# Optimization experiments

Hardware: AMD Instinct MI355X
Metric: run time of the kernel (lower is better)

The kernel has to match this reference:

```python
import jax, jax.numpy as jnp
import numpy as np

B, T = 256, 128
DW = 768          # dim_word
DH = 768          # dim_hidden (must equal DW per broadcast in original code)
NC = 3            # num_classification
VOCAB = 50000
TVOCAB = 5000


def setup_inputs() -> dict:
    key = jax.random.key(0)
    ks = jax.random.split(key, 16)
    u = 1.0 / np.sqrt(DH)
    uni = lambda k, shape: jax.random.uniform(k, shape, jnp.float32, -u, u)
    inp = {
        'sent': jax.random.randint(ks[0], (B, T), 0, VOCAB),
        'target': jax.random.randint(ks[1], (B,), 0, TVOCAB),
        'lens': jnp.clip(jax.random.randint(ks[2], (B,), 0, T + 1), 1, T),
        'emb': jax.random.normal(ks[3], (VOCAB, DW), jnp.float32) * 0.1,
        'temb': jax.random.normal(ks[4], (TVOCAB, DW), jnp.float32) * 0.1,
        # LSTM cell params: input = cat(x_t, target_x) -> 2*DW
        'W_ih': uni(ks[5], (2 * DW, 4 * DH)),
        'W_hh': uni(ks[6], (DH, 4 * DH)),
        'b_lstm': uni(ks[7], (4 * DH,)),
        'Wh': uni(ks[8], (DH, DH)),
        'Wv': uni(ks[9], (DW, DW)),
        'w': uni(ks[10], (DH + DW,)),
        'Wp': uni(ks[11], (DH, DH)),
        'Wx': uni(ks[12], (DH, DH)),
        'W_lin': uni(ks[13], (DH, NC)),
        'b_lin': uni(ks[14], (NC,)),
    }
    return inp


def _forward(sent, target, lens, emb, temb, W_ih, W_hh, b_lstm, Wh, Wv, w, Wp, Wx, W_lin, b_lin):
    x = emb[sent]                      # [B, T, DW]
    tx = temb[target]                  # [B, DW]
    mask = (jnp.arange(T)[None, :] < lens[:, None]).astype(x.dtype)  # [B, T]

    def step(carry, ins):
        h, c = carry
        xt, mt = ins                   # [B, DW], [B]
        inp = jnp.concatenate([xt, tx], axis=-1)          # [B, 2*DW]
        gates = inp @ W_ih + h @ W_hh + b_lstm            # [B, 4*DH]
        i, f, g, o = jnp.split(gates, 4, axis=-1)
        c_new = jax.nn.sigmoid(f) * c + jax.nn.sigmoid(i) * jnp.tanh(g)
        h_new = jax.nn.sigmoid(o) * jnp.tanh(c_new)
        m = mt[:, None]
        h = m * h_new + (1.0 - m) * h   # mask blend (hold state past seq end)
        c = m * c_new + (1.0 - m) * c
        return (h, c), h

    h0 = jnp.zeros((x.shape[0], DH), x.dtype)
    c0 = jnp.zeros((x.shape[0], DH), x.dtype)
    xs = (jnp.swapaxes(x, 0, 1), mask.T)                 # time-major
    _, Hs = jax.lax.scan(step, (h0, c0), xs)
    H = jnp.swapaxes(Hs, 0, 1)                            # [B, T, DH]

    # attention: M = tanh([H Wh ; aspect Wv]); scores = M @ w, masked softmax
    aspect_proj = (tx @ Wv)[:, None, :]                   # [B, 1, DW] broadcast over T
    M = jnp.tanh(jnp.concatenate(
        [H @ Wh, jnp.broadcast_to(aspect_proj, H.shape)], axis=-1))  # [B, T, DH+DW]
    scores = M @ w                                        # [B, T]
    scores = jnp.where(mask > 0, scores, -1e9)
    alpha = jax.nn.softmax(scores, axis=-1)               # [B, T]
    r = jnp.einsum('bt,btd->bd', alpha, H)                # [B, DH]
    h_star = jnp.tanh(r @ Wp + H[:, -1, :] @ Wx)          # [B, DH]
    # dropout is identity in eval mode
    logit = h_star @ W_lin + b_lin                        # [B, NC]
    return logit


def reference(sent, target, lens, emb, temb, W_ih, W_hh, b_lstm, Wh, Wv, w, Wp, Wx, W_lin, b_lin):
    return _forward(sent, target, lens, emb, temb, W_ih, W_hh, b_lstm,
                    Wh, Wv, w, Wp, Wx, W_lin, b_lin)
```

## Files before the change

### kernel.cpp

```cpp
#include <hip/hip_runtime.h>
#include <stdint.h>

#define Bz 256
#define Tz 128
#define DWz 768
#define DHz 768
#define G4z 3072
#define NBLK 96
#define NGRID 256

typedef __attribute__((ext_vector_type(8))) short short8;
typedef __attribute__((ext_vector_type(4))) float f32x4;
typedef __attribute__((ext_vector_type(4))) int i32x4;

__device__ __forceinline__ unsigned short f2bf(float x) {
    union { float f; unsigned int u; } v; v.f = x;
    unsigned int u = v.u;
    return (unsigned short)((u + 0x7fffu + ((u >> 16) & 1u)) >> 16);
}
__device__ __forceinline__ float bf2f(unsigned short h) {
    union { unsigned int u; float f; } v; v.u = ((unsigned int)h) << 16;
    return v.f;
}
__device__ __forceinline__ float fsigm(float x) {
    return __builtin_amdgcn_rcpf(1.0f + __builtin_amdgcn_exp2f(x * -1.4426950408889634f));
}
__device__ __forceinline__ float ftanh(float x) {
    x = fminf(fmaxf(x, -15.0f), 15.0f);
    float e = __builtin_amdgcn_exp2f(x * -2.8853900817779268f);
    return (1.0f - e) * __builtin_amdgcn_rcpf(1.0f + e);
}

__global__ __launch_bounds__(256) void k_prep_wswz(const float* __restrict__ W,
                                                   unsigned short* __restrict__ out, int NT) {
    __shared__ float sT[32][132];
    int bid = blockIdx.x;
    int kt = bid / NT, nt = bid - kt * NT;
    int tid = threadIdx.x;
    int ldn = NT * 128;
    {
        int r = tid >> 3;
        int cb = (tid & 7) * 16;
        const float* src = W + (long)(kt * 32 + r) * ldn + nt * 128 + cb;
#pragma unroll
        for (int u = 0; u < 4; ++u) {
            float4 v = ((const float4*)src)[u];
            sT[r][cb + u * 4 + 0] = v.x; sT[r][cb + u * 4 + 1] = v.y;
            sT[r][cb + u * 4 + 2] = v.z; sT[r][cb + u * 4 + 3] = v.w;
        }
    }
    __syncthreads();
#pragma unroll
    for (int it = 0; it < 2; ++it) {
        int s = tid + it * 256;
        int n = s >> 2, kq = s & 3;
        alignas(16) unsigned short o[8];
#pragma unroll
        for (int e = 0; e < 8; ++e) o[e] = f2bf(sT[kq * 8 + e][n]);
        *(int4*)(out + ((long)bid * 512 + s) * 8) = *(const int4*)o;
    }
}

__global__ __launch_bounds__(256) void k_prep_whh(const float* __restrict__ Whh,
                                                  unsigned short* __restrict__ WhhP) {
    __shared__ float sT[32][65];
    int bid = blockIdx.x;
    int dblk = bid / 24;
    int k0c = bid - dblk * 24;
    int tid = threadIdx.x;
    {
        int kk = tid >> 3;
        int seg = tid & 7;
        const float* src = Whh + (long)(k0c * 32 + kk) * G4z
                         + (seg >> 1) * 768 + dblk * 16 + (seg & 1) * 8;
        float4 v0 = *(const float4*)src;
        float4 v1 = *(const float4*)(src + 4);
        int cl = seg * 8;
        sT[kk][cl + 0] = v0.x; sT[kk][cl + 1] = v0.y; sT[kk][cl + 2] = v0.z; sT[kk][cl + 3] = v0.w;
        sT[kk][cl + 4] = v1.x; sT[kk][cl + 5] = v1.y; sT[kk][cl + 6] = v1.z; sT[kk][cl + 7] = v1.w;
    }
    __syncthreads();
    {
        int nl = tid >> 2, cc = tid & 3;
        int q8 = cc ^ ((nl >> 1) & 3);
        int clv = (nl >> 4) * 16 + (nl & 15);
        alignas(16) unsigned short o[8];
#pragma unroll
        for (int e = 0; e < 8; ++e) o[e] = f2bf(sT[q8 * 8 + e][clv]);
        *(int4*)(WhhP + (long)(dblk * 6144 + k0c * 256 + tid) * 8) = *(const int4*)o;
    }
}

__global__ __launch_bounds__(256) void k_gemm_cg(const int* __restrict__ target,
                                                 const float* __restrict__ temb,
                                                 const unsigned short* __restrict__ WbP,
                                                 const float* __restrict__ bias,
                                                 float* __restrict__ C) {
    __shared__ unsigned short sA[128 * 40];
    __shared__ unsigned short sB[128 * 40];
    int tid = threadIdx.x;
    int n0 = blockIdx.x * 128;
    int m0 = blockIdx.y * 128;
    int wid = tid >> 6, lane = tid & 63, l15 = lane & 15, q = lane >> 4;
    int wm = wid >> 1, wn = wid & 1;
    int arow = tid >> 1;
    int kp = (tid & 1) * 16;
    long gbase = (long)target[m0 + arow] * DWz;
    int s0 = tid, s1 = tid + 256;
    int bd0 = (s0 >> 2) * 40 + (((s0 & 3) ^ (((s0 >> 2) >> 3) & 3)) << 3);
    int bd1 = (s1 >> 2) * 40 + (((s1 & 3) ^ (((s1 >> 2) >> 3) & 3)) << 3);

    f32x4 acc[4][4];
    f32x4 zz = {0.f, 0.f, 0.f, 0.f};
#pragma unroll
    for (int i = 0; i < 4; ++i)
#pragma unroll
        for (int j = 0; j < 4; ++j) acc[i][j] = zz;

    for (int k0 = 0; k0 < DWz; k0 += 32) {
        {
            const float* src = temb + gbase + k0 + kp;
            alignas(16) unsigned short tmp[16];
#pragma unroll
            for (int it = 0; it < 4; ++it) {
                float4 v = ((const float4*)src)[it];
                tmp[it * 4 + 0] = f2bf(v.x); tmp[it * 4 + 1] = f2bf(v.y);
                tmp[it * 4 + 2] = f2bf(v.z); tmp[it * 4 + 3] = f2bf(v.w);
            }
            *(int4*)(sA + arow * 40 + kp) = *(const int4*)tmp;
            *(int4*)(sA + arow * 40 + kp + 8) = *(const int4*)(tmp + 8);
        }
        {
            const int4* wsrc = (const int4*)WbP
                + ((long)((k0 >> 5) * 24 + (n0 >> 7))) * 512 + tid;
            int4 v0 = wsrc[0];
            int4 v1 = wsrc[256];
            *(int4*)(sB + bd0) = v0;
            *(int4*)(sB + bd1) = v1;
        }
        __syncthreads();
        short8 af[4], bfr[4];
#pragma unroll
        for (int i = 0; i < 4; ++i)
            af[i] = *(const short8*)(sA + (wm * 64 + i * 16 + l15) * 40 + q * 8);
#pragma unroll
        for (int j = 0; j < 4; ++j) {
            int n = wn * 64 + j * 16 + l15;
            bfr[j] = *(const short8*)(sB + n * 40 + ((q ^ ((n >> 3) & 3)) << 3));
        }
#pragma unroll
        for (int i = 0; i < 4; ++i)
#pragma unroll
            for (int j = 0; j < 4; ++j)
                acc[i][j] = __builtin_amdgcn_mfma_f32_16x16x32_bf16(af[i], bfr[j], acc[i][j], 0, 0, 0);
        __syncthreads();
    }
#pragma unroll
    for (int i = 0; i < 4; ++i)
#pragma unroll
        for (int j = 0; j < 4; ++j) {
            int col = n0 + wn * 64 + j * 16 + l15;
            float bv = bias[col];
#pragma unroll
            for (int r = 0; r < 4; ++r) {
                int row = m0 + wm * 64 + i * 16 + q * 4 + r;
                C[(long)row * G4z + col] = acc[i][j][r] + bv;
            }
        }
}

__global__ __launch_bounds__(256) void k_gemm_x(const float* __restrict__ emb,
                                                const int* __restrict__ sent,
                                                const unsigned short* __restrict__ WbP,
                                                unsigned short* __restrict__ xW) {
    __shared__ unsigned short sA[128 * 40];
    __shared__ unsigned short sB[128 * 40];
    int tid = threadIdx.x;
    int n0 = blockIdx.x * 128;
    int m0 = blockIdx.y * 128;
    int wid = tid >> 6, lane = tid & 63, l15 = lane & 15, q = lane >> 4;
    int wm = wid >> 1, wn = wid & 1;
    int arow = tid >> 1;
    int kp = (tid & 1) * 16;
    int m = m0 + arow;
    int tt = m >> 8;
    int bb = m & 255;
    long gbase = (long)sent[bb * Tz + tt] * DWz;
    int s0 = tid, s1 = tid + 256;
    int bd0 = (s0 >> 2) * 40 + (((s0 & 3) ^ (((s0 >> 2) >> 3) & 3)) << 3);
    int bd1 = (s1 >> 2) * 40 + (((s1 & 3) ^ (((s1 >> 2) >> 3) & 3)) << 3);

    f32x4 acc[4][4];
    f32x4 zz = {0.f, 0.f, 0.f, 0.f};
#pragma unroll
    for (int i = 0; i < 4; ++i)
#pragma unroll
        for (int j = 0; j < 4; ++j) acc[i][j] = zz;

    for (int k0 = 0; k0 < DWz; k0 += 32) {
        {
            const float* src = emb + gbase + k0 + kp;
            alignas(16) unsigned short tmp[16];
#pragma unroll
            for (int it = 0; it < 4; ++it) {
                float4 v = ((const float4*)src)[it];
                tmp[it * 4 + 0] = f2bf(v.x); tmp[it * 4 + 1] = f2bf(v.y);
                tmp[it * 4 + 2] = f2bf(v.z); tmp[it * 4 + 3] = f2bf(v.w);
            }
            *(int4*)(sA + arow * 40 + kp) = *(const int4*)tmp;
            *(int4*)(sA + arow * 40 + kp + 8) = *(const int4*)(tmp + 8);
        }
        {
            const int4* wsrc = (const int4*)WbP
                + ((long)((k0 >> 5) * 24 + (n0 >> 7))) * 512 + tid;
            int4 v0 = wsrc[0];
            int4 v1 = wsrc[256];
            *(int4*)(sB + bd0) = v0;
            *(int4*)(sB + bd1) = v1;
        }
        __syncthreads();
        short8 af[4], bfr[4];
#pragma unroll
        for (int i = 0; i < 4; ++i)
            af[i] = *(const short8*)(sA + (wm * 64 + i * 16 + l15) * 40 + q * 8);
#pragma unroll
        for (int j = 0; j < 4; ++j) {
            int n = wn * 64 + j * 16 + l15;
            bfr[j] = *(const short8*)(sB + n * 40 + ((q ^ ((n >> 3) & 3)) << 3));
        }
#pragma unroll
        for (int i = 0; i < 4; ++i)
#pragma unroll
            for (int j = 0; j < 4; ++j)
                acc[i][j] = __builtin_amdgcn_mfma_f32_16x16x32_bf16(af[i], bfr[j], acc[i][j], 0, 0, 0);
        __syncthreads();
    }
#pragma unroll
    for (int j = 0; j < 4; ++j) {
        int n = n0 + wn * 64 + j * 16 + l15;
        int gt = n / 768;
        int dblk = (n - gt * 768) >> 4;
#pragma unroll
        for (int ip = 0; ip < 2; ++ip) {
            int row = m0 + wm * 64 + ip * 32;
            int t = row >> 8;
            int bq = (row & 255) + q * 4;
            int blk = dblk * 2 + (bq >> 7);
            int tidd = ((bq & 127) >> 5) * 64 + q * 16 + l15;
            alignas(16) unsigned short o[8];
#pragma unroll
            for (int r = 0; r < 4; ++r) {
                o[r]     = f2bf(acc[ip * 2][j][r]);
                o[4 + r] = f2bf(acc[ip * 2 + 1][j][r]);
            }
            *(int4*)(xW + (((long)t * 96 + blk) * 4 + gt) * 2048 + (long)tidd * 8) = *(const int4*)o;
        }
    }
}

#define UNPACK(PF, G)                                                        \
    {                                                                        \
        const unsigned short* ch_ = (const unsigned short*)&(PF);            \
        _Pragma("unroll")                                                    \
        for (int i_ = 0; i_ < 2; ++i_)                                       \
            _Pragma("unroll")                                                \
            for (int r_ = 0; r_ < 4; ++r_)                                   \
                xg[i_][G][r_] = bf2f(ch_[i_ * 4 + r_]) + xgc[i_][G][r_];     \
    }

__global__ __launch_bounds__(256, 1) void k_lstm_all(int t0, int t1,
        unsigned short* __restrict__ xW, const float* __restrict__ constg,
        const unsigned short* __restrict__ WhhP, unsigned short* __restrict__ Hbf,
        float* __restrict__ cbuf, const int* __restrict__ lens,
        unsigned* __restrict__ bar, unsigned* __restrict__ xwcnt, int waitxw,
        const float* __restrict__ emb, const int* __restrict__ sent,
        const unsigned short* __restrict__ WihbP, int nprod) {
    extern __shared__ unsigned short sB[];
    int bid = blockIdx.x;
    int tid = threadIdx.x;
    int lane = tid & 63, wid = tid >> 6;
    int l15 = lane & 15, q = lane >> 4;

    if (bid >= NBLK) {
        unsigned short* psA = sB;
        unsigned short* psB = sB + 5120;
        int wm = wid >> 1, wn = wid & 1;
        int arow = tid >> 1;
        int kp = (tid & 1) * 16;
        int s0 = tid, s1 = tid + 256;
        int bd0 = (s0 >> 2) * 40 + (((s0 & 3) ^ (((s0 >> 2) >> 3) & 3)) << 3);
        int bd1 = (s1 >> 2) * 40 + (((s1 & 3) ^ (((s1 >> 2) >> 3) & 3)) << 3);

        for (int g = bid - NBLK; g < 6144; g += nprod) {
            int my = g / 24, nx = g - (g / 24) * 24;
            int m0 = my * 128, n0 = nx * 128;
            int m = m0 + arow;
            int tt = m >> 8, bb2 = m & 255;
            long gbase = (long)sent[bb2 * Tz + tt] * DWz;

            f32x4 acc[4][4];
            f32x4 zz = {0.f, 0.f, 0.f, 0.f};
#pragma unroll
            for (int i = 0; i < 4; ++i)
#pragma unroll
                for (int j = 0; j < 4; ++j) acc[i][j] = zz;

            for (int k0 = 0; k0 < DWz; k0 += 32) {
                {
                    const float* src = emb + gbase + k0 + kp;
                    alignas(16) unsigned short tmp[16];
#pragma unroll
                    for (int it = 0; it < 4; ++it) {
                        float4 v = ((const float4*)src)[it];
                        tmp[it * 4 + 0] = f2bf(v.x); tmp[it * 4 + 1] = f2bf(v.y);
                        tmp[it * 4 + 2] = f2bf(v.z); tmp[it * 4 + 3] = f2bf(v.w);
                    }
                    *(int4*)(psA + arow * 40 + kp) = *(const int4*)tmp;
                    *(int4*)(psA + arow * 40 + kp + 8) = *(const int4*)(tmp + 8);
                }
                {
                    const int4* wsrc = (const int4*)WihbP
                        + ((long)((k0 >> 5) * 24 + (n0 >> 7))) * 512 + tid;
                    int4 v0 = wsrc[0];
                    int4 v1 = wsrc[256];
                    *(int4*)(psB + bd0) = v0;
                    *(int4*)(psB + bd1) = v1;
                }
                __syncthreads();
                short8 af[4], bfr[4];
#pragma unroll
                for (int i = 0; i < 4; ++i)
                    af[i] = *(const short8*)(psA + (wm * 64 + i * 16 + l15) * 40 + q * 8);
#pragma unroll
                for (int j = 0; j < 4; ++j) {
                    int n = wn * 64 + j * 16 + l15;
                    bfr[j] = *(const short8*)(psB + n * 40 + ((q ^ ((n >> 3) & 3)) << 3));
                }
#pragma unroll
                for (int i = 0; i < 4; ++i)
#pragma unroll
                    for (int j = 0; j < 4; ++j)
                        acc[i][j] = __builtin_amdgcn_mfma_f32_16x16x32_bf16(af[i], bfr[j], acc[i][j], 0, 0, 0);
                __syncthreads();
            }
#pragma unroll
            for (int j = 0; j < 4; ++j) {
                int n = n0 + wn * 64 + j * 16 + l15;
                int gt = n / 768;
                int dblk2 = (n - gt * 768) >> 4;
#pragma unroll
                for (int ip = 0; ip < 2; ++ip) {
                    int row = m0 + wm * 64 + ip * 32;
                    int t = row >> 8;
                    int bq = (row & 255) + q * 4;
                    int blk = dblk2 * 2 + (bq >> 7);
                    int tidd = ((bq & 127) >> 5) * 64 + q * 16 + l15;
                    alignas(16) unsigned short o[8];
#pragma unroll
                    for (int r = 0; r < 4; ++r) {
                        o[r]     = f2bf(acc[ip * 2][j][r]);
                        o[4 + r] = f2bf(acc[ip * 2 + 1][j][r]);
                    }
                    unsigned long long* dst = (unsigned long long*)
                        (xW + (((long)t * 96 + blk) * 4 + gt) * 2048 + (long)tidd * 8);
                    const unsigned long long* po = (const unsigned long long*)o;
                    __hip_atomic_store(dst, po[0], __ATOMIC_RELAXED, __HIP_MEMORY_SCOPE_AGENT);
                    __hip_atomic_store(dst + 1, po[1], __ATOMIC_RELAXED, __HIP_MEMORY_SCOPE_AGENT);
                }
            }
            asm volatile("s_waitcnt vmcnt(0)" ::: "memory");
            __syncthreads();
            if (tid == 0)
                (void)__hip_atomic_fetch_add(&xwcnt[(my >> 1) * 32], 1u,
                                             __ATOMIC_RELAXED, __HIP_MEMORY_SCOPE_AGENT);
        }
        return;
    }

    int bm = bid & 1;
    int dblk = bid >> 1;
    int d0 = dblk * 16;
    int d = d0 + l15;
    unsigned* flg = bar + ((bm * 4 + wid) * 48) * 32;

    {
        const int4* src = (const int4*)WhhP + (long)dblk * 6144;
        for (int s = tid; s < 6144; s += 256) ((int4*)sB)[s] = src[s];
    }

    int brow[8];
    int lenr[8];
    float c[8], h[8];
    float xgc[2][4][4];
#pragma unroll
    for (int i = 0; i < 2; ++i)
#pragma unroll
        for (int r = 0; r < 4; ++r) {
            int ir = i * 4 + r;
            int b = bm * 128 + wid * 32 + i * 16 + q * 4 + r;
            brow[ir] = b;
            lenr[ir] = lens[b];
            long cbase = (long)b * G4z + d;
#pragma unroll
            for (int j = 0; j < 4; ++j) xgc[i][j][r] = constg[cbase + j * 768];
            if (t0 > 0) {
                c[ir] = cbuf[(long)b * DHz + d];
                h[ir] = bf2f(Hbf[((long)b * Tz + (t0 - 1)) * DHz + d]);
            } else { c[ir] = 0.f; h[ir] = 0.f; }
        }

    int bbase[4];
#pragma unroll
    for (int j = 0; j < 4; ++j) {
        int nl = j * 16 + l15;
        bbase[j] = nl * 32 + ((q ^ ((nl >> 1) & 3)) << 3);
    }
    __syncthreads();

    if (waitxw) {
        const unsigned* xc = xwcnt + t0 * 32;
        if (lane == 0)
            while (__hip_atomic_load(xc, __ATOMIC_RELAXED, __HIP_MEMORY_SCOPE_AGENT) < 48u)
                __builtin_amdgcn_s_sleep(1);
        asm volatile("" ::: "memory");
    }
    float xg[2][4][4];
    {
        const unsigned short* x0 = xW + ((long)t0 * 96 + bid) * 8192 + (long)tid * 8;
        int4 c0 = *(const int4*)(x0);
        int4 c1 = *(const int4*)(x0 + 2048);
        int4 c2 = *(const int4*)(x0 + 4096);
        int4 c3 = *(const int4*)(x0 + 6144);
        UNPACK(c0, 0) UNPACK(c1, 1) UNPACK(c2, 2) UNPACK(c3, 3)
    }

    i32x4 pf0, pf1, pf2, pf3;

    for (int t = t0; t < t1; ++t) {
        if (t > t0) {
            unsigned tgt = (unsigned)t;
            const unsigned* fp = flg + lane * 32;
            while (true) {
                unsigned v = (lane < 48)
                    ? __hip_atomic_load(fp, __ATOMIC_RELAXED, __HIP_MEMORY_SCOPE_AGENT)
                    : tgt;
                if (__all(v >= tgt)) break;
                __builtin_amdgcn_s_sleep(1);
            }
            asm volatile("s_waitcnt vmcnt(0)" ::: "memory");
            __builtin_amdgcn_sched_barrier(0);
            UNPACK(pf0, 0) UNPACK(pf1, 1) UNPACK(pf2, 2) UNPACK(pf3, 3)
        }

        f32x4 acc[2][4];
        f32x4 zz = {0.f, 0.f, 0.f, 0.f};
#pragma unroll
        for (int i = 0; i < 2; ++i)
#pragma unroll
            for (int j = 0; j < 4; ++j) acc[i][j] = zz;

        if (t > 0) {
            const unsigned short* ap0 = Hbf + ((long)(bm * 128 + wid * 32 + l15) * Tz + (t - 1)) * DHz + q * 8;
            const unsigned short* ap1 = ap0 + (long)16 * Tz * DHz;
#pragma unroll 6
            for (int k0c = 0; k0c < 24; ++k0c) {
                short8 a0 = *(const short8*)(ap0 + k0c * 32);
                short8 a1 = *(const short8*)(ap1 + k0c * 32);
                const unsigned short* bb = sB + k0c * 2048;
#pragma unroll
                for (int j = 0; j < 4; ++j) {
                    short8 bf = *(const short8*)(bb + bbase[j]);
                    acc[0][j] = __builtin_amdgcn_mfma_f32_16x16x32_bf16(a0, bf, acc[0][j], 0, 0, 0);
                    acc[1][j] = __builtin_amdgcn_mfma_f32_16x16x32_bf16(a1, bf, acc[1][j], 0, 0, 0);
                }
            }
        }

#pragma unroll
        for (int i = 0; i < 2; ++i)
#pragma unroll
            for (int r = 0; r < 4; ++r) {
                int ir = i * 4 + r;
                float gi = acc[i][0][r] + xg[i][0][r];
                float gf = acc[i][1][r] + xg[i][1][r];
                float gg = acc[i][2][r] + xg[i][2][r];
                float go = acc[i][3][r] + xg[i][3][r];
                float cn = fsigm(gf) * c[ir] + fsigm(gi) * ftanh(gg);
                float hn = fsigm(go) * ftanh(cn);
                bool upd = t < lenr[ir];
                c[ir] = upd ? cn : c[ir];
                h[ir] = upd ? hn : h[ir];
                __hip_atomic_store(Hbf + ((long)brow[ir] * Tz + t) * DHz + d, f2bf(h[ir]),
                                   __ATOMIC_RELAXED, __HIP_MEMORY_SCOPE_AGENT);
            }

        if (t + 1 < t1) {
            if (waitxw) {
                const unsigned* xc = xwcnt + (t + 1) * 32;
                if (lane == 0)
                    while (__hip_atomic_load(xc, __ATOMIC_RELAXED, __HIP_MEMORY_SCOPE_AGENT) < 48u)
                        __builtin_amdgcn_s_sleep(1);
                asm volatile("" ::: "memory");
            }
            const unsigned short* pp = xW + ((long)(t + 1) * 96 + bid) * 8192 + (long)tid * 8;
            asm volatile(
                "global_load_dwordx4 %0, %4, off\n\t"
                "global_load_dwordx4 %1, %5, off\n\t"
                "global_load_dwordx4 %2, %6, off\n\t"
                "global_load_dwordx4 %3, %7, off"
                : "=&v"(pf0), "=&v"(pf1), "=&v"(pf2), "=&v"(pf3)
                : "v"(pp), "v"(pp + 2048), "v"(pp + 4096), "v"(pp + 6144)
                : "memory");
            asm volatile("s_waitcnt vmcnt(4)" ::: "memory");
            if (lane == 0)
                __hip_atomic_store(flg + dblk * 32, (unsigned)(t + 1),
                                   __ATOMIC_RELAXED, __HIP_MEMORY_SCOPE_AGENT);
        }
    }
#pragma unroll
    for (int ir = 0; ir < 8; ++ir) cbuf[(long)brow[ir] * DHz + d] = c[ir];
}

__global__ __launch_bounds__(256) void k_scores(const unsigned short* __restrict__ Hbf,
                                                const unsigned short* __restrict__ WbP,
                                                const float* __restrict__ wv,
                                                float* __restrict__ scores) {
    __shared__ unsigned short sA[128 * 40];
    __shared__ unsigned short sB[128 * 40];
    __shared__ float sred[128];
    int tid = threadIdx.x;
    int n0 = blockIdx.x * 128;
    int m0 = blockIdx.y * 128;
    int wid = tid >> 6, lane = tid & 63, l15 = lane & 15, q = lane >> 4;
    int wm = wid >> 1, wn = wid & 1;

    int s0 = tid, s1 = tid + 256;
    int bd0 = (s0 >> 2) * 40 + (((s0 & 3) ^ (((s0 >> 2) >> 3) & 3)) << 3);
    int bd1 = (s1 >> 2) * 40 + (((s1 & 3) ^ (((s1 >> 2) >> 3) & 3)) << 3);

    f32x4 acc[4][4];
    f32x4 zz = {0.f, 0.f, 0.f, 0.f};
#pragma unroll
    for (int i = 0; i < 4; ++i)
#pragma unroll
        for (int j = 0; j < 4; ++j) acc[i][j] = zz;

    int arow = tid >> 1;
    int kp = (tid & 1) * 16;
    const unsigned short* asrc = Hbf + (long)(m0 + arow) * DHz;

    for (int k0 = 0; k0 < DHz; k0 += 32) {
        *(int4*)(sA + arow * 40 + kp) = *(const int4*)(asrc + k0 + kp);
        *(int4*)(sA + arow * 40 + kp + 8) = *(const int4*)(asrc + k0 + kp + 8);
        {
            const int4* wsrc = (const int4*)WbP
                + ((long)((k0 >> 5) * 6 + (n0 >> 7))) * 512 + tid;
            int4 v0 = wsrc[0];
            int4 v1 = wsrc[256];
            *(int4*)(sB + bd0) = v0;
            *(int4*)(sB + bd1) = v1;
        }
        __syncthreads();
        short8 af[4], bfr[4];
#pragma unroll
        for (int i = 0; i < 4; ++i)
            af[i] = *(const short8*)(sA + (wm * 64 + i * 16 + l15) * 40 + q * 8);
#pragma unroll
        for (int j = 0; j < 4; ++j) {
            int n = wn * 64 + j * 16 + l15;
            bfr[j] = *(const short8*)(sB + n * 40 + ((q ^ ((n >> 3) & 3)) << 3));
        }
#pragma unroll
        for (int i = 0; i < 4; ++i)
#pragma unroll
            for (int j = 0; j < 4; ++j)
                acc[i][j] = __builtin_amdgcn_mfma_f32_16x16x32_bf16(af[i], bfr[j], acc[i][j], 0, 0, 0);
        __syncthreads();
    }
    if (tid < 128) sred[tid] = 0.f;
    __syncthreads();
#pragma unroll
    for (int i = 0; i < 4; ++i)
#pragma unroll
        for (int r = 0; r < 4; ++r) {
            float sv = 0.f;
#pragma unroll
            for (int j = 0; j < 4; ++j) {
                int n = n0 + wn * 64 + j * 16 + l15;
                sv += ftanh(acc[i][j][r]) * wv[n];
            }
#pragma unroll
            for (int o = 1; o < 16; o <<= 1) sv += __shfl_xor(sv, o, 64);
            if (l15 == 0) atomicAdd(&sred[wm * 64 + i * 16 + q * 4 + r], sv);
        }
    __syncthreads();
    if (tid < 128) atomicAdd(&scores[m0 + tid], sred[tid]);
}

__global__ __launch_bounds__(128) void k_attn(const float* __restrict__ scores,
                                              const int* __restrict__ lens,
                                              const unsigned short* __restrict__ Hbf,
                                              float* __restrict__ rbuf) {
    int b = blockIdx.x, t = threadIdx.x;
    __shared__ float sal[Tz];
    __shared__ float rA[2], rB[2];
    int len = lens[b];
    float s = (t < len) ? scores[b * Tz + t] : -1e9f;
    float m = s;
#pragma unroll
    for (int o = 32; o; o >>= 1) m = fmaxf(m, __shfl_xor(m, o, 64));
    if ((t & 63) == 0) rA[t >> 6] = m;
    __syncthreads();
    m = fmaxf(rA[0], rA[1]);
    float e = expf(s - m);
    float sum = e;
#pragma unroll
    for (int o = 32; o; o >>= 1) sum += __shfl_xor(sum, o, 64);
    if ((t & 63) == 0) rB[t >> 6] = sum;
    __syncthreads();
    sum = rB[0] + rB[1];
    sal[t] = e / sum;
    __syncthreads();
    if (t < 96) {
        const unsigned short* hp = Hbf + (long)b * Tz * DHz + t * 8;
        float acc[8] = {};
        for (int tt = 0; tt < Tz; ++tt) {
            short8 v = *(const short8*)(hp + (long)tt * DHz);
            float a = sal[tt];
            const unsigned short* pv = (const unsigned short*)&v;
#pragma unroll
            for (int e2 = 0; e2 < 8; ++e2) acc[e2] += a * bf2f(pv[e2]);
        }
        float* rp = rbuf + (long)b * DHz + t * 8;
#pragma unroll
        for (int e2 = 0; e2 < 8; ++e2) rp[e2] = acc[e2];
    }
}

__global__ __launch_bounds__(256) void k_hstar(const float* __restrict__ rbuf,
                                               const unsigned short* __restrict__ Hbf,
                                               const unsigned short* __restrict__ WbP,
                                               float* __restrict__ hst) {
    __shared__ unsigned short sA[128 * 40];
    __shared__ unsigned short sB[128 * 40];
    int tid = threadIdx.x;
    int n0 = blockIdx.x * 128;
    int m0 = blockIdx.y * 128;
    int wid = tid >> 6, lane = tid & 63, l15 = lane & 15, q = lane >> 4;
    int wm = wid >> 1, wn = wid & 1;
    int arow = tid >> 1;
    int kp = (tid & 1) * 16;
    int s0 = tid, s1 = tid + 256;
    int bd0 = (s0 >> 2) * 40 + (((s0 & 3) ^ (((s0 >> 2) >> 3) & 3)) << 3);
    int bd1 = (s1 >> 2) * 40 + (((s1 & 3) ^ (((s1 >> 2) >> 3) & 3)) << 3);

    f32x4 acc[4][4];
    f32x4 zz = {0.f, 0.f, 0.f, 0.f};
#pragma unroll
    for (int i = 0; i < 4; ++i)
#pragma unroll
        for (int j = 0; j < 4; ++j) acc[i][j] = zz;

    for (int k0 = 0; k0 < 2 * DHz; k0 += 32) {
        if (k0 < DHz) {
            const float* src = rbuf + (long)(m0 + arow) * DHz + k0 + kp;
            alignas(16) unsigned short tmp[16];
#pragma unroll
            for (int it = 0; it < 4; ++it) {
                float4 v = ((const float4*)src)[it];
                tmp[it * 4 + 0] = f2bf(v.x); tmp[it * 4 + 1] = f2bf(v.y);
                tmp[it * 4 + 2] = f2bf(v.z); tmp[it * 4 + 3] = f2bf(v.w);
            }
            *(int4*)(sA + arow * 40 + kp) = *(const int4*)tmp;
            *(int4*)(sA + arow * 40 + kp + 8) = *(const int4*)(tmp + 8);
        } else {
            const unsigned short* src = Hbf + ((long)(m0 + arow) * Tz + (Tz - 1)) * DHz
                                      + (k0 - DHz) + kp;
            *(int4*)(sA + arow * 40 + kp) = *(const int4*)src;
            *(int4*)(sA + arow * 40 + kp + 8) = *(const int4*)(src + 8);
        }
        {
            const int4* wsrc = (const int4*)WbP
                + ((long)((k0 >> 5) * 6 + (n0 >> 7))) * 512 + tid;
            int4 v0 = wsrc[0];
            int4 v1 = wsrc[256];
            *(int4*)(sB + bd0) = v0;
            *(int4*)(sB + bd1) = v1;
        }
        __syncthreads();
        short8 af[4], bfr[4];
#pragma unroll
        for (int i = 0; i < 4; ++i)
            af[i] = *(const short8*)(sA + (wm * 64 + i * 16 + l15) * 40 + q * 8);
#pragma unroll
        for (int j = 0; j < 4; ++j) {
            int n = wn * 64 + j * 16 + l15;
            bfr[j] = *(const short8*)(sB + n * 40 + ((q ^ ((n >> 3) & 3)) << 3));
        }
#pragma unroll
        for (int i = 0; i < 4; ++i)
#pragma unroll
            for (int j = 0; j < 4; ++j)
                acc[i][j] = __builtin_amdgcn_mfma_f32_16x16x32_bf16(af[i], bfr[j], acc[i][j], 0, 0, 0);
        __syncthreads();
    }
#pragma unroll
    for (int i = 0; i < 4; ++i)
#pragma unroll
        for (int j = 0; j < 4; ++j) {
            int col = n0 + wn * 64 + j * 16 + l15;
#pragma unroll
            for (int r = 0; r < 4; ++r) {
                int row = m0 + wm * 64 + i * 16 + q * 4 + r;
                hst[(long)row * DHz + col] = ftanh(acc[i][j][r]);
            }
        }
}

__global__ void k_logits(const float* __restrict__ hst, const float* __restrict__ Wl,
                         const float* __restrict__ bl, float* __restrict__ out) {
    int b = blockIdx.x;
    int lane = threadIdx.x & 63, c = threadIdx.x >> 6;
    float s = 0.f;
    for (int k = lane; k < DHz; k += 64) s += hst[(long)b * DHz + k] * Wl[k * 3 + c];
#pragma unroll
    for (int o = 32; o; o >>= 1) s += __shfl_xor(s, o, 64);
    if (lane == 0) out[b * 3 + c] = s + bl[c];
}

extern "C" void kernel_launch(void* const* d_in, const int* in_sizes, int n_in,
                              void* d_out, int out_size, void* d_ws, size_t ws_size,
                              hipStream_t stream) {
    (void)in_sizes; (void)n_in; (void)out_size; (void)ws_size;
    const int*   sent   = (const int*)d_in[0];
    const int*   target = (const int*)d_in[1];
    const int*   lens   = (const int*)d_in[2];
    const float* emb    = (const float*)d_in[3];
    const float* temb   = (const float*)d_in[4];
    const float* W_ih   = (const float*)d_in[5];
    const float* W_hh   = (const float*)d_in[6];
    const float* b_lstm = (const float*)d_in[7];
    const float* Wh     = (const float*)d_in[8];
    const float* wv     = (const float*)d_in[10];
    const float* Wp     = (const float*)d_in[11];
    const float* Wx     = (const float*)d_in[12];
    const float* W_lin  = (const float*)d_in[13];
    const float* b_lin  = (const float*)d_in[14];
    float* out = (float*)d_out;

    char* ws = (char*)d_ws;
    size_t off = 0;
    auto alloc = [&](size_t bytes) -> void* {
        void* p = ws + off;
        off = (off + bytes + 255) & ~(size_t)255;
        return p;
    };
    unsigned short* xW    = (unsigned short*)alloc((size_t)32768 * G4z * 2);
    unsigned short* Hbf   = (unsigned short*)alloc((size_t)Bz * Tz * DHz * 2);
    unsigned short* WihbP = (unsigned short*)alloc((size_t)24 * 24 * 512 * 16);
    unsigned short* Wih2P = (unsigned short*)alloc((size_t)24 * 24 * 512 * 16);
    unsigned short* WhhP  = (unsigned short*)alloc((size_t)48 * 6144 * 16);
    unsigned short* WhbP  = (unsigned short*)alloc((size_t)24 * 6 * 512 * 16);
    unsigned short* WpxP  = (unsigned short*)alloc((size_t)48 * 6 * 512 * 16);
    float* constg = (float*)alloc((size_t)Bz * G4z * 4);
    float* cbuf   = (float*)alloc((size_t)Bz * DHz * 4);
    float* scores = (float*)alloc((size_t)Bz * Tz * 4);
    float* rbuf   = (float*)alloc((size_t)Bz * DHz * 4);
    float* hst    = (float*)alloc((size_t)Bz * DHz * 4);
    unsigned* bar = (unsigned*)alloc(65536);
    unsigned* xwc = (unsigned*)alloc(16384);

    k_prep_wswz<<<576, 256, 0, stream>>>(W_ih, WihbP, 24);
    k_prep_wswz<<<576, 256, 0, stream>>>(W_ih + (size_t)DWz * G4z, Wih2P, 24);
    k_prep_wswz<<<144, 256, 0, stream>>>(Wh, WhbP, 6);
    k_prep_wswz<<<144, 256, 0, stream>>>(Wp, WpxP, 6);
    k_prep_wswz<<<144, 256, 0, stream>>>(Wx, WpxP + (size_t)144 * 512 * 8, 6);
    k_prep_whh<<<1152, 256, 0, stream>>>(W_hh, WhhP);
    hipMemsetAsync(scores, 0, (size_t)Bz * Tz * 4, stream);
    hipMemsetAsync(bar, 0, 65536, stream);
    hipMemsetAsync(xwc, 0, 16384, stream);

    k_gemm_cg<<<dim3(24, 2), 256, 0, stream>>>(target, temb, Wih2P, b_lstm, constg);

    hipFuncSetAttribute((const void*)k_lstm_all,
                        hipFuncAttributeMaxDynamicSharedMemorySize, 98304);
    int t0v = 0, t1v = Tz, waitv = 1, nprodv = NGRID - NBLK;
    unsigned short* xWp = xW;
    const float* cgp = constg;
    const unsigned short* whp = WhhP;
    unsigned short* hbp = Hbf;
    float* cbp = cbuf;
    const int* lnp = lens;
    unsigned* barp = bar;
    unsigned* xwcp = xwc;
    const float* embp = emb;
    const int* sentp = sent;
    const unsigned short* wihp = WihbP;
    void* kargs[] = {&t0v, &t1v, &xWp, &cgp, &whp, &hbp, &cbp, &lnp, &barp,
                     &xwcp, &waitv, &embp, &sentp, &wihp, &nprodv};
    hipError_t ce = hipLaunchCooperativeKernel(reinterpret_cast<void*>(k_lstm_all),
                                               dim3(NGRID), dim3(256), kargs, 98304, stream);
    if (ce != hipSuccess) {
        k_gemm_x<<<dim3(24, 256), 256, 0, stream>>>(emb, sent, WihbP, xW);
        for (int t = 0; t < Tz; ++t)
            k_lstm_all<<<NBLK, 256, 98304, stream>>>(t, t + 1, xW, constg, WhhP, Hbf,
                                                     cbuf, lens, bar, xwc, 0,
                                                     emb, sent, WihbP, 0);
    }

    k_scores<<<dim3(6, 256), 256, 0, stream>>>(Hbf, WhbP, wv, scores);
    k_attn<<<Bz, 128, 0, stream>>>(scores, lens, Hbf, rbuf);
    k_hstar<<<dim3(6, 2), 256, 0, stream>>>(rbuf, Hbf, WpxP, hst);
    k_logits<<<Bz, 192, 0, stream>>>(hst, W_lin, b_lin, out);
}
```

Before: 1.909 ms.

## Overlap attention score GEMM with LSTM recurrence inside persistent kernel

Producer blocks of the cooperative LSTM kernel, once their input-projection GEMM work is finished, now compute the H@Wh tanh and dot-with-w attention scores per timestep. Each waits on the per-block step flags until that timestep's hidden states are published, then accumulates into scores with atomics. This takes the separate k_scores launch off the serial tail and hides it behind the recurrence. The five weight-prep launches are also merged into one kernel. The cost is extra flag polling traffic and atomic accumulation, plus some risk of contention with the recurrent blocks.

After: 1.858 ms. -2.6%, faster.

```diff
diff --git a/kernel.cpp b/kernel.cpp
--- a/kernel.cpp
+++ b/kernel.cpp
@@ -31,11 +31,23 @@
     return (1.0f - e) * __builtin_amdgcn_rcpf(1.0f + e);
 }
 
-__global__ __launch_bounds__(256) void k_prep_wswz(const float* __restrict__ W,
-                                                   unsigned short* __restrict__ out, int NT) {
+__global__ __launch_bounds__(256) void k_prep_all(const float* __restrict__ W_ih,
+                                                  const float* __restrict__ Wh,
+                                                  const float* __restrict__ Wp,
+                                                  const float* __restrict__ Wx,
+                                                  unsigned short* __restrict__ WihbP,
+                                                  unsigned short* __restrict__ Wih2P,
+                                                  unsigned short* __restrict__ WhbP,
+                                                  unsigned short* __restrict__ WpxP) {
     __shared__ float sT[32][132];
     int bid = blockIdx.x;
-    int kt = bid / NT, nt = bid - kt * NT;
+    const float* W; unsigned short* out; int NT, rb;
+    if (bid < 576)       { W = W_ih;                        out = WihbP; NT = 24; rb = bid; }
+    else if (bid < 1152) { W = W_ih + (size_t)DWz * G4z;    out = Wih2P; NT = 24; rb = bid - 576; }
+    else if (bid < 1296) { W = Wh;                          out = WhbP;  NT = 6;  rb = bid - 1152; }
+    else if (bid < 1440) { W = Wp;                          out = WpxP;  NT = 6;  rb = bid - 1296; }
+    else                 { W = Wx; out = WpxP + (size_t)144 * 512 * 8;   NT = 6;  rb = bid - 1440; }
+    int kt = rb / NT, nt = rb - kt * NT;
     int tid = threadIdx.x;
     int ldn = NT * 128;
     {
@@ -57,7 +69,7 @@
         alignas(16) unsigned short o[8];
 #pragma unroll
         for (int e = 0; e < 8; ++e) o[e] = f2bf(sT[kq * 8 + e][n]);
-        *(int4*)(out + ((long)bid * 512 + s) * 8) = *(const int4*)o;
+        *(int4*)(out + ((long)rb * 512 + s) * 8) = *(const int4*)o;
     }
 }
 
@@ -274,7 +286,9 @@
         float* __restrict__ cbuf, const int* __restrict__ lens,
         unsigned* __restrict__ bar, unsigned* __restrict__ xwcnt, int waitxw,
         const float* __restrict__ emb, const int* __restrict__ sent,
-        const unsigned short* __restrict__ WihbP, int nprod) {
+        const unsigned short* __restrict__ WihbP, int nprod,
+        const unsigned short* __restrict__ WhbP, const float* __restrict__ wv,
+        float* __restrict__ scores) {
     extern __shared__ unsigned short sB[];
     int bid = blockIdx.x;
     int tid = threadIdx.x;
@@ -284,6 +298,7 @@
     if (bid >= NBLK) {
         unsigned short* psA = sB;
         unsigned short* psB = sB + 5120;
+        float* sred = (float*)(sB + 10240);
         int wm = wid >> 1, wn = wid & 1;
         int arow = tid >> 1;
         int kp = (tid & 1) * 16;
@@ -374,6 +389,84 @@
                 (void)__hip_atomic_fetch_add(&xwcnt[(my >> 1) * 32], 1u,
                                              __ATOMIC_RELAXED, __HIP_MEMORY_SCOPE_AGENT);
         }
+
+        for (int s2 = bid - NBLK; s2 < 1536; s2 += nprod) {
+            int t = s2 / 12;
+            int rr = s2 - t * 12;
+            int mt = rr / 6, nt2 = rr - (rr / 6) * 6;
+            int m0 = mt * 128, n0 = nt2 * 128;
+            unsigned tgt = (unsigned)(t + 1);
+            {
+                const unsigned* fp2 = bar + (((mt * 4 + wid) * 48) + lane) * 32;
+                while (true) {
+                    unsigned v = (lane < 48)
+                        ? __hip_atomic_load(fp2, __ATOMIC_RELAXED, __HIP_MEMORY_SCOPE_AGENT)
+                        : tgt;
+                    if (__all(v >= tgt)) break;
+                    __builtin_amdgcn_s_sleep(8);
+                }
+            }
+            __syncthreads();
+
+            f32x4 acc[4][4];
+            f32x4 zz = {0.f, 0.f, 0.f, 0.f};
+#pragma unroll
+            for (int i = 0; i < 4; ++i)
+#pragma unroll
+                for (int j = 0; j < 4; ++j) acc[i][j] = zz;
+
+            for (int k0 = 0; k0 < DHz; k0 += 32) {
+                {
+                    const unsigned short* asrc = Hbf
+                        + ((long)(m0 + arow) * Tz + t) * DHz + k0 + kp;
+                    *(int4*)(psA + arow * 40 + kp) = *(const int4*)asrc;
+                    *(int4*)(psA + arow * 40 + kp + 8) = *(const int4*)(asrc + 8);
+                }
+                {
+                    const int4* wsrc = (const int4*)WhbP
+                        + ((long)((k0 >> 5) * 6 + nt2)) * 512 + tid;
+                    int4 v0 = wsrc[0];
+                    int4 v1 = wsrc[256];
+                    *(int4*)(psB + bd0) = v0;
+                    *(int4*)(psB + bd1) = v1;
+                }
+                __syncthreads();
+                short8 af[4], bfr[4];
+#pragma unroll
+                for (int i = 0; i < 4; ++i)
+                    af[i] = *(const short8*)(psA + (wm * 64 + i * 16 + l15) * 40 + q * 8);
+#pragma unroll
+                for (int j = 0; j < 4; ++j) {
+                    int n = wn * 64 + j * 16 + l15;
+                    bfr[j] = *(const short8*)(psB + n * 40 + ((q ^ ((n >> 3) & 3)) << 3));
+                }
+#pragma unroll
+                for (int i = 0; i < 4; ++i)
+#pragma unroll
+                    for (int j = 0; j < 4; ++j)
+                        acc[i][j] = __builtin_amdgcn_mfma_f32_16x16x32_bf16(af[i], bfr[j], acc[i][j], 0, 0, 0);
+                __syncthreads();
+            }
+            if (tid < 128) sred[tid] = 0.f;
+            __syncthreads();
+#pragma unroll
+            for (int i = 0; i < 4; ++i)
+#pragma unroll
+                for (int r = 0; r < 4; ++r) {
+                    float sv = 0.f;
+#pragma unroll
+                    for (int j = 0; j < 4; ++j) {
+                        int n = n0 + wn * 64 + j * 16 + l15;
+                        sv += ftanh(acc[i][j][r]) * wv[n];
+                    }
+#pragma unroll
+                    for (int o = 1; o < 16; o <<= 1) sv += __shfl_xor(sv, o, 64);
+                    if (l15 == 0) atomicAdd(&sred[wm * 64 + i * 16 + q * 4 + r], sv);
+                }
+            __syncthreads();
+            if (tid < 128)
+                atomicAdd(&scores[(long)(m0 + tid) * Tz + t], sred[tid]);
+        }
         return;
     }
 
@@ -517,6 +610,10 @@
                                    __ATOMIC_RELAXED, __HIP_MEMORY_SCOPE_AGENT);
         }
     }
+    asm volatile("s_waitcnt vmcnt(0)" ::: "memory");
+    if (lane == 0)
+        __hip_atomic_store(flg + dblk * 32, (unsigned)t1,
+                           __ATOMIC_RELAXED, __HIP_MEMORY_SCOPE_AGENT);
 #pragma unroll
     for (int ir = 0; ir < 8; ++ir) cbuf[(long)brow[ir] * DHz + d] = c[ir];
 }
@@ -770,11 +867,7 @@
     unsigned* bar = (unsigned*)alloc(65536);
     unsigned* xwc = (unsigned*)alloc(16384);
 
-    k_prep_wswz<<<576, 256, 0, stream>>>(W_ih, WihbP, 24);
-    k_prep_wswz<<<576, 256, 0, stream>>>(W_ih + (size_t)DWz * G4z, Wih2P, 24);
-    k_prep_wswz<<<144, 256, 0, stream>>>(Wh, WhbP, 6);
-    k_prep_wswz<<<144, 256, 0, stream>>>(Wp, WpxP, 6);
-    k_prep_wswz<<<144, 256, 0, stream>>>(Wx, WpxP + (size_t)144 * 512 * 8, 6);
+    k_prep_all<<<1584, 256, 0, stream>>>(W_ih, Wh, Wp, Wx, WihbP, Wih2P, WhbP, WpxP);
     k_prep_whh<<<1152, 256, 0, stream>>>(W_hh, WhhP);
     hipMemsetAsync(scores, 0, (size_t)Bz * Tz * 4, stream);
     hipMemsetAsync(bar, 0, 65536, stream);
@@ -796,8 +889,12 @@
     const float* embp = emb;
     const int* sentp = sent;
     const unsigned short* wihp = WihbP;
+    const unsigned short* whbp = WhbP;
+    const float* wvp = wv;
+    float* scp = scores;
     void* kargs[] = {&t0v, &t1v, &xWp, &cgp, &whp, &hbp, &cbp, &lnp, &barp,
-                     &xwcp, &waitv, &embp, &sentp, &wihp, &nprodv};
+                     &xwcp, &waitv, &embp, &sentp, &wihp, &nprodv,
+                     &whbp, &wvp, &scp};
     hipError_t ce = hipLaunchCooperativeKernel(reinterpret_cast<void*>(k_lstm_all),
                                                dim3(NGRID), dim3(256), kargs, 98304, stream);
     if (ce != hipSuccess) {
@@ -805,10 +902,11 @@
         for (int t = 0; t < Tz; ++t)
             k_lstm_all<<<NBLK, 256, 98304, stream>>>(t, t + 1, xW, constg, WhhP, Hbf,
                                                      cbuf, lens, bar, xwc, 0,
-                                                     emb, sent, WihbP, 0);
-    }
-
-    k_scores<<<dim3(6, 256), 256, 0, stream>>>(Hbf, WhbP, wv, scores);
+                                                     emb, sent, WihbP, 0,
+                                                     WhbP, wv, scores);
+        k_scores<<<dim3(6, 256), 256, 0, stream>>>(Hbf, WhbP, wv, scores);
+    }
+
     k_attn<<<Bz, 128, 0, stream>>>(scores, lens, Hbf, rbuf);
     k_hstar<<<dim3(6, 2), 256, 0, stream>>>(rbuf, Hbf, WpxP, hst);
     k_logits<<<Bz, 192, 0, stream>>>(hst, W_lin, b_lin, out);
```
